# Performance work log

Measured on AMD Instinct MI355X. Metric: run time of the kernel, lower is better.

## Reference

```python
import jax, jax.numpy as jnp
import numpy as np

BN_EPS = 1e-5
DIST_EPS = 1e-8


def setup_inputs() -> dict:
    key = jax.random.key(0)
    ks = jax.random.split(key, 8)
    B, N, S = 8, 8192, 2048
    D_unk, D_kn = 128, 256
    inp = {
        "unknown_xyz": jax.random.uniform(ks[0], (B, N, 3), dtype=jnp.float32),
        "known_xyz": jax.random.uniform(ks[1], (B, S, 3), dtype=jnp.float32),
        "unknown_points": jax.random.normal(ks[2], (B, N, D_unk), dtype=jnp.float32),
        "known_points": jax.random.normal(ks[3], (B, S, D_kn), dtype=jnp.float32),
        "W0": jax.random.normal(ks[4], (256, 384), dtype=jnp.float32) * (1.0 / np.sqrt(384)),
        "b0": jnp.zeros((256,), jnp.float32),
        "g0": jnp.ones((256,), jnp.float32),
        "beta0": jnp.zeros((256,), jnp.float32),
        "W1": jax.random.normal(ks[5], (128, 256), dtype=jnp.float32) * (1.0 / np.sqrt(256)),
        "b1": jnp.zeros((128,), jnp.float32),
        "g1": jnp.ones((128,), jnp.float32),
        "beta1": jnp.zeros((128,), jnp.float32),
    }
    return inp


def _three_nn(unknown_xyz, known_xyz):
    # squared pairwise distances [B, N, S]
    d = jnp.sum((unknown_xyz[:, :, None, :] - known_xyz[:, None, :, :]) ** 2, axis=-1)
    neg_top, idx = jax.lax.top_k(-d, 3)  # 3 smallest distances
    return -neg_top, idx  # dists [B,N,3], idx [B,N,3]


def _conv_bn_relu(x, W, b, g, beta):
    # x: [B, N, Cin]; 1x1 Conv1d == per-point linear
    y = jnp.einsum("bnc,oc->bno", x, W) + b
    mean = jnp.mean(y, axis=(0, 1))
    var = jnp.var(y, axis=(0, 1))  # biased, as BatchNorm training forward
    y = g * (y - mean) * jax.lax.rsqrt(var + BN_EPS) + beta
    return jax.nn.relu(y)


def reference(unknown_xyz, known_xyz, unknown_points, known_points,
              W0, b0, g0, beta0, W1, b1, g1, beta1):
    dists, idx = _three_nn(unknown_xyz, known_xyz)
    dist_recip = 1.0 / (dists + DIST_EPS)
    weight = dist_recip / jnp.sum(dist_recip, axis=2, keepdims=True)  # [B,N,3]
    # gather 3 neighbor features: [B,N,3,D_kn]
    gathered = jax.vmap(lambda f, i: f[i])(known_points, idx)
    interpolated = jnp.sum(weight[..., None] * gathered, axis=2)  # [B,N,D_kn]
    x = jnp.concatenate([unknown_points, interpolated], axis=-1)  # [B,N,384]
    x = _conv_bn_relu(x, W0, b0, g0, beta0)
    x = _conv_bn_relu(x, W1, b1, g1, beta1)
    return x  # [B, N, 128]
```

## Files before the change

kernel.cpp:

```cpp
#include <hip/hip_runtime.h>
#include <hip/hip_bf16.h>


typedef __attribute__((ext_vector_type(8))) short short8;
typedef __attribute__((ext_vector_type(4))) float f32x4;

#define BB 8
#define NN 8192
#define SS 2048
#define M_TOT (BB * NN)
#define N1DIM 256
#define K2DIM 256
#define N2DIM 128
#define BK 64

#define GDIM 5
#define NCELL (GDIM * GDIM * GDIM)
#define SLOTS 32
#define CELLW 0.2f

#define KEY_MASK 0xFFFFF800u
#define IDX_MASK 0x7FFu

__device__ __forceinline__ unsigned short f2bf(float f) {
    unsigned int x = __float_as_uint(f);
    unsigned int r = x + 0x7fffu + ((x >> 16) & 1u);
    return (unsigned short)(r >> 16);
}
__device__ __forceinline__ float bf2f(unsigned short u) {
    return __uint_as_float(((unsigned int)u) << 16);
}
__device__ __forceinline__ unsigned int med3_u32(unsigned int a, unsigned int b,
                                                 unsigned int c) {
    unsigned int r;
    asm("v_med3_u32 %0, %1, %2, %3" : "=v"(r) : "v"(a), "v"(b), "v"(c));
    return r;
}

__device__ __forceinline__ void ins5(unsigned int k[5], unsigned int key) {
    unsigned int n1 = med3_u32(k[0], k[1], key);
    unsigned int n2 = med3_u32(k[1], k[2], key);
    unsigned int n3 = med3_u32(k[2], k[3], key);
    unsigned int n4 = med3_u32(k[3], k[4], key);
    k[0] = min(k[0], key);
    k[1] = n1; k[2] = n2; k[3] = n3; k[4] = n4;
}

__device__ __forceinline__ float rescue_write(
    const unsigned int k[5], float qx, float qy, float qz,
    const float4* __restrict__ kpB, uint4* __restrict__ widx, size_t pt)
{
    unsigned long long e[5];
#pragma unroll
    for (int i = 0; i < 5; ++i) {
        if ((k[i] & KEY_MASK) >= 0x7F800000u) {
            e[i] = 0xFFFFFFFFFFFFFFFFull;
        } else {
            unsigned int idx = k[i] & IDX_MASK;
            float4 c = kpB[idx];
            float dx = c.x - qx, dy = c.y - qy, dz = c.z - qz;
            float d = fmaf(dx, dx, fmaf(dy, dy, dz * dz));
            e[i] = ((unsigned long long)__float_as_uint(d) << 32) | idx;
        }
    }
#pragma unroll
    for (int i = 0; i < 3; ++i)
#pragma unroll
        for (int j = i + 1; j < 5; ++j)
            if (e[j] < e[i]) { unsigned long long t = e[i]; e[i] = e[j]; e[j] = t; }

    float d0 = __uint_as_float((unsigned int)(e[0] >> 32));
    float d1 = __uint_as_float((unsigned int)(e[1] >> 32));
    float d2 = __uint_as_float((unsigned int)(e[2] >> 32));
    float r0 = 1.0f / (d0 + 1e-8f);
    float r1 = 1.0f / (d1 + 1e-8f);
    float r2 = 1.0f / (d2 + 1e-8f);
    float rs = 1.0f / (r0 + r1 + r2);
    unsigned int i0 = (unsigned int)(e[0] & IDX_MASK);
    unsigned int i1 = (unsigned int)(e[1] & IDX_MASK);
    unsigned int i2 = (unsigned int)(e[2] & IDX_MASK);
    widx[pt] = make_uint4(__float_as_uint(r0 * rs), __float_as_uint(r1 * rs),
                          i0 | (i1 << 16), i2);
    return d2;
}

__device__ __forceinline__ void gload_lds16(const void* g, void* lds) {
    __builtin_amdgcn_global_load_lds(
        (const __attribute__((address_space(1))) unsigned int*)g,
        (__attribute__((address_space(3))) unsigned int*)lds, 16, 0, 0);
}

__global__ __launch_bounds__(256) void cvt_w_kernel(
    const float* __restrict__ W0, const float* __restrict__ W1,
    const float* __restrict__ kxyz,
    unsigned short* __restrict__ Wa, unsigned short* __restrict__ Wb,
    unsigned short* __restrict__ Wb1, float4* __restrict__ kpack,
    float4* __restrict__ table, int* __restrict__ cnt,
    int* __restrict__ nfail, float* __restrict__ statsF)
{
    int i = blockIdx.x * 256 + threadIdx.x;
    if (blockIdx.x == 0) {
        for (int j = threadIdx.x; j < 4608; j += 256) statsF[j] = 0.0f;
        if (threadIdx.x == 0) *nfail = 0;
    }
    if (i < BB * NCELL) cnt[i] = 0;
    if (i < BB * NCELL * SLOTS)
        table[i] = make_float4(1e30f, 1e30f, 1e30f, 0.0f);
    if (i < 256 * 384) {
        int o = i / 384, c = i - o * 384;
        unsigned short v = f2bf(W0[i]);
        if (c < 128) Wa[o * 128 + c] = v;
        else         Wb[o * 256 + (c - 128)] = v;
    }
    if (i < N2DIM * K2DIM) Wb1[i] = f2bf(W1[i]);
    if (i < BB * SS) {
        const float* p = kxyz + (size_t)i * 3;
        float px = p[0], py = p[1], pz = p[2];
        kpack[i] = make_float4(px, py, pz, fmaf(px, px, fmaf(py, py, pz * pz)));
    }
}

__global__ __launch_bounds__(256) void bin_scatter_kernel(
    const float* __restrict__ kxyz, float4* __restrict__ table,
    int* __restrict__ cnt)
{
    int i = blockIdx.x * 256 + threadIdx.x;
    if (i >= BB * SS) return;
    int b = i >> 11, s = i & 2047;
    const float* p = kxyz + (size_t)i * 3;
    float x = p[0], y = p[1], z = p[2];
    int cx = min((int)(x * GDIM), GDIM - 1);
    int cy = min((int)(y * GDIM), GDIM - 1);
    int cz = min((int)(z * GDIM), GDIM - 1);
    int cell = (cz * GDIM + cy) * GDIM + cx;
    int slot = atomicAdd(&cnt[b * NCELL + cell], 1);
    if (slot < SLOTS)
        table[((size_t)(b * NCELL + cell)) * SLOTS + slot] =
            make_float4(x, y, z, __int_as_float(s));
}

__global__ __launch_bounds__(256) void nn_grid_kernel(
    const float* __restrict__ uxyz, const float4* __restrict__ table,
    const int* __restrict__ cnt, const float4* __restrict__ kpack,
    uint4* __restrict__ widx, int* __restrict__ fail_list,
    int* __restrict__ nfail)
{
    const int t  = blockIdx.x * 256 + threadIdx.x;
    const int qd = t & 3;
    const size_t pt = (size_t)(t >> 2);
    const int b = (int)(pt >> 13);

    const float* up = uxyz + pt * 3;
    const float qx = up[0], qy = up[1], qz = up[2];

    const int cx = min((int)(qx * GDIM), GDIM - 1);
    const int cy = min((int)(qy * GDIM), GDIM - 1);
    const int cz = min((int)(qz * GDIM), GDIM - 1);
    const float fx = qx * GDIM - cx, fy = qy * GDIM - cy, fz = qz * GDIM - cz;
    int ox = cx - (fx <= 0.5f ? 1 : 0); ox = max(0, min(ox, GDIM - 2));
    int oy = cy - (fy <= 0.5f ? 1 : 0); oy = max(0, min(oy, GDIM - 2));
    int oz = cz - (fz <= 0.5f ? 1 : 0); oz = max(0, min(oz, GDIM - 2));

    const float4* tb = table + (size_t)b * NCELL * SLOTS;
    const int* cb = cnt + b * NCELL;

    unsigned int k[5] = {0xFFFFFFFFu, 0xFFFFFFFFu, 0xFFFFFFFFu,
                         0xFFFFFFFFu, 0xFFFFFFFFu};
    int ovf = 0;
#pragma unroll
    for (int jj = 0; jj < 2; ++jj) {
        const int j = qd * 2 + jj;
        const int dx = j & 1, dy = (j >> 1) & 1, dz = j >> 2;
        const int cell = ((oz + dz) * GDIM + (oy + dy)) * GDIM + (ox + dx);
        ovf |= (cb[cell] > SLOTS) ? 1 : 0;
        const float4* cp = tb + (size_t)cell * SLOTS;
#pragma unroll 8
        for (int s = 0; s < SLOTS; ++s) {
            float4 c = cp[s];
            float ddx = c.x - qx, ddy = c.y - qy, ddz = c.z - qz;
            float d = fmaf(ddx, ddx, fmaf(ddy, ddy, ddz * ddz));
            unsigned int key = (__float_as_uint(d) & KEY_MASK) |
                               (unsigned int)__float_as_int(c.w);
            ins5(k, key);
        }
    }

#pragma unroll
    for (int m = 1; m <= 2; m <<= 1) {
        unsigned int f0 = (unsigned int)__shfl_xor((int)k[0], m);
        unsigned int f1 = (unsigned int)__shfl_xor((int)k[1], m);
        unsigned int f2 = (unsigned int)__shfl_xor((int)k[2], m);
        unsigned int f3 = (unsigned int)__shfl_xor((int)k[3], m);
        unsigned int f4 = (unsigned int)__shfl_xor((int)k[4], m);
        ovf |= __shfl_xor(ovf, m);
        ins5(k, f0); ins5(k, f1); ins5(k, f2); ins5(k, f3); ins5(k, f4);
    }

    if (qd != 0) return;

    float d3 = rescue_write(k, qx, qy, qz, kpack + (size_t)b * SS, widx, pt);

    float lx = ox * CELLW, rx = (ox + 2) * CELLW;
    float ly = oy * CELLW, ry = (oy + 2) * CELLW;
    float lz = oz * CELLW, rz = (oz + 2) * CELLW;
    float covx = fminf(ox == 0 ? 1e30f : qx - lx, ox == GDIM - 2 ? 1e30f : rx - qx);
    float covy = fminf(oy == 0 ? 1e30f : qy - ly, oy == GDIM - 2 ? 1e30f : ry - qy);
    float covz = fminf(oz == 0 ? 1e30f : qz - lz, oz == GDIM - 2 ? 1e30f : rz - qz);
    float g = fminf(covx, fminf(covy, covz));

    if (ovf || !(d3 <= g * g)) {
        int pos = atomicAdd(nfail, 1);
        fail_list[pos] = (int)pt;
    }
}

__global__ __launch_bounds__(256) void nn_brute_kernel(
    const float* __restrict__ uxyz, const float4* __restrict__ kpack,
    const int* __restrict__ fail_list, const int* __restrict__ nfail,
    uint4* __restrict__ widx)
{
    const int l = threadIdx.x & 63;
    const int wv = (blockIdx.x * 256 + threadIdx.x) >> 6;
    const int nw = (gridDim.x * 256) >> 6;
    const int n = *nfail;

    for (int q = wv; q < n; q += nw) {
        const size_t pt = (size_t)fail_list[q];
        const int b = (int)(pt >> 13);
        const float* up = uxyz + pt * 3;
        const float qx = up[0], qy = up[1], qz = up[2];
        const float4* kp = kpack + (size_t)b * SS;

        unsigned int k[5] = {0xFFFFFFFFu, 0xFFFFFFFFu, 0xFFFFFFFFu,
                             0xFFFFFFFFu, 0xFFFFFFFFu};
#pragma unroll 4
        for (int s = l; s < SS; s += 64) {
            float4 c = kp[s];
            float ddx = c.x - qx, ddy = c.y - qy, ddz = c.z - qz;
            float d = fmaf(ddx, ddx, fmaf(ddy, ddy, ddz * ddz));
            unsigned int key = (__float_as_uint(d) & KEY_MASK) | (unsigned int)s;
            ins5(k, key);
        }
#pragma unroll
        for (int m = 1; m <= 32; m <<= 1) {
            unsigned int f0 = (unsigned int)__shfl_xor((int)k[0], m);
            unsigned int f1 = (unsigned int)__shfl_xor((int)k[1], m);
            unsigned int f2 = (unsigned int)__shfl_xor((int)k[2], m);
            unsigned int f3 = (unsigned int)__shfl_xor((int)k[3], m);
            unsigned int f4 = (unsigned int)__shfl_xor((int)k[4], m);
            ins5(k, f0); ins5(k, f1); ins5(k, f2); ins5(k, f3); ins5(k, f4);
        }
        if (l == 0)
            rescue_write(k, qx, qy, qz, kp, widx, pt);
    }
}

__global__ __launch_bounds__(512, 4) void zgemm_kernel(
    const float* __restrict__ kpts,
    const unsigned short* __restrict__ Wb,
    unsigned short* __restrict__ Z)
{
    __shared__ __align__(128) unsigned char smem[2 * 32768];

    const int tid = threadIdx.x;
    const int l = tid & 63, w = tid >> 6;
    const int wm = w >> 2, wn = w & 3;
    const int mt = blockIdx.x >> 1, nh = blockIdx.x & 1;
    const int row0 = mt * 128;
    const int srow = l >> 3, sbo = (l & 7) * 16;
    const int lr = tid >> 2, lcq = tid & 3;

    f32x4 acc[4][2];
#pragma unroll
    for (int m = 0; m < 4; ++m)
#pragma unroll
        for (int n = 0; n < 2; ++n) {
            f32x4 z = {0.f, 0.f, 0.f, 0.f};
            acc[m][n] = z;
        }

    const unsigned char* Bb = (const unsigned char*)Wb + (size_t)nh * 128 * 512;
    float4 af0, af1, af2, af3;

    auto issueA = [&](int t) {
        const float* src = kpts + (size_t)(row0 + lr) * 256 + t * 64 + lcq * 16;
        af0 = ((const float4*)src)[0];
        af1 = ((const float4*)src)[1];
        af2 = ((const float4*)src)[2];
        af3 = ((const float4*)src)[3];
    };
    auto stageB = [&](int buf, int t) {
        unsigned char* Bl = smem + buf * 32768 + 16384;
#pragma unroll
        for (int i = 0; i < 2; ++i) {
            const int r = w * 16 + i * 8 + srow;
            gload_lds16(Bb + (size_t)r * 512 + t * 128 + (sbo ^ ((r & 7) << 4)),
                        Bl + r * 128 + sbo);
        }
    };
    auto xformA = [&](int buf) {
        unsigned char* Al = smem + buf * 32768;
        short8 o0, o1;
        o0[0] = (short)f2bf(af0.x); o0[1] = (short)f2bf(af0.y);
        o0[2] = (short)f2bf(af0.z); o0[3] = (short)f2bf(af0.w);
        o0[4] = (short)f2bf(af1.x); o0[5] = (short)f2bf(af1.y);
        o0[6] = (short)f2bf(af1.z); o0[7] = (short)f2bf(af1.w);
        o1[0] = (short)f2bf(af2.x); o1[1] = (short)f2bf(af2.y);
        o1[2] = (short)f2bf(af2.z); o1[3] = (short)f2bf(af2.w);
        o1[4] = (short)f2bf(af3.x); o1[5] = (short)f2bf(af3.y);
        o1[6] = (short)f2bf(af3.z); o1[7] = (short)f2bf(af3.w);
        const int bo = lcq * 32;
        *(short8*)(Al + lr * 128 + ((bo) ^ ((lr & 7) << 4))) = o0;
        *(short8*)(Al + lr * 128 + ((bo + 16) ^ ((lr & 7) << 4))) = o1;
    };
    auto compute = [&](int buf) {
        const unsigned char* Al = smem + buf * 32768;
        const unsigned char* Bl = Al + 16384;
#pragma unroll
        for (int ks = 0; ks < 2; ++ks) {
            const int bo = ks * 64 + (l >> 4) * 16;
            short8 a[4], bq[2];
#pragma unroll
            for (int m = 0; m < 4; ++m) {
                const int r = wm * 64 + m * 16 + (l & 15);
                a[m] = *(const short8*)(Al + r * 128 + (bo ^ ((r & 7) << 4)));
            }
#pragma unroll
            for (int n = 0; n < 2; ++n) {
                const int r = wn * 32 + n * 16 + (l & 15);
                bq[n] = *(const short8*)(Bl + r * 128 + (bo ^ ((r & 7) << 4)));
            }
#pragma unroll
            for (int m = 0; m < 4; ++m)
#pragma unroll
                for (int n = 0; n < 2; ++n)
                    acc[m][n] = __builtin_amdgcn_mfma_f32_16x16x32_bf16(
                        a[m], bq[n], acc[m][n], 0, 0, 0);
        }
    };

    issueA(0);
    stageB(0, 0);
    xformA(0);
    __syncthreads();
#pragma unroll
    for (int t = 0; t < 4; ++t) {
        const int cur = t & 1;
        if (t + 1 < 4) { issueA(t + 1); stageB(cur ^ 1, t + 1); }
        compute(cur);
        if (t + 1 < 4) xformA(cur ^ 1);
        __syncthreads();
    }

#pragma unroll
    for (int m = 0; m < 4; ++m) {
        const int row = row0 + wm * 64 + m * 16 + (l >> 4) * 4;
#pragma unroll
        for (int n = 0; n < 2; ++n) {
            const int col = nh * 128 + wn * 32 + n * 16 + (l & 15);
            f32x4 v = acc[m][n];
#pragma unroll
            for (int r = 0; r < 4; ++r)
                Z[(size_t)(row + r) * 256 + col] = f2bf(v[r]);
        }
    }
}

__global__ __launch_bounds__(512, 4) void gemm1u_kernel(
    const float* __restrict__ upts,
    const unsigned short* __restrict__ Wa,
    unsigned short* __restrict__ Y0u)
{
    __shared__ __align__(128) unsigned char smem[65536];

    const int tid = threadIdx.x;
    const int l = tid & 63, w = tid >> 6;
    const int wm = w >> 2, wn = w & 3;
    const int mt = blockIdx.x >> 1, nh = blockIdx.x & 1;
    const int row0 = mt * 128;
    const int srow = l >> 3, sbo = (l & 7) * 16;
    const int lr = tid >> 2, lcq = tid & 3;

    {
        const unsigned char* Bb = (const unsigned char*)Wa + (size_t)nh * 128 * 256;
#pragma unroll
        for (int h = 0; h < 2; ++h)
#pragma unroll
            for (int i = 0; i < 2; ++i) {
                const int r = w * 16 + i * 8 + srow;
                gload_lds16(Bb + (size_t)r * 256 + h * 128 + (sbo ^ ((r & 7) << 4)),
                            smem + 32768 + h * 16384 + r * 128 + sbo);
            }
    }
    {
        const float* src = upts + (size_t)(row0 + lr) * 128 + lcq * 32;
        float4 f[8];
#pragma unroll
        for (int q = 0; q < 8; ++q) f[q] = ((const float4*)src)[q];
        unsigned char* Ah = smem + (lcq >> 1) * 16384;
        const int cb = (lcq & 1) * 64;
#pragma unroll
        for (int q = 0; q < 4; ++q) {
            float4 fa = f[q * 2], fb = f[q * 2 + 1];
            short8 o;
            o[0] = (short)f2bf(fa.x); o[1] = (short)f2bf(fa.y);
            o[2] = (short)f2bf(fa.z); o[3] = (short)f2bf(fa.w);
            o[4] = (short)f2bf(fb.x); o[5] = (short)f2bf(fb.y);
            o[6] = (short)f2bf(fb.z); o[7] = (short)f2bf(fb.w);
            *(short8*)(Ah + lr * 128 + ((cb + q * 16) ^ ((lr & 7) << 4))) = o;
        }
    }
    __syncthreads();

    f32x4 acc[4][2];
#pragma unroll
    for (int m = 0; m < 4; ++m)
#pragma unroll
        for (int n = 0; n < 2; ++n) {
            f32x4 z = {0.f, 0.f, 0.f, 0.f};
            acc[m][n] = z;
        }
#pragma unroll
    for (int ks = 0; ks < 4; ++ks) {
        const unsigned char* Al = smem + (ks >> 1) * 16384;
        const unsigned char* Bl = smem + 32768 + (ks >> 1) * 16384;
        const int bo = (ks & 1) * 64 + (l >> 4) * 16;
        short8 a[4], bq[2];
#pragma unroll
        for (int m = 0; m < 4; ++m) {
            const int r = wm * 64 + m * 16 + (l & 15);
            a[m] = *(const short8*)(Al + r * 128 + (bo ^ ((r & 7) << 4)));
        }
#pragma unroll
        for (int n = 0; n < 2; ++n) {
            const int r = wn * 32 + n * 16 + (l & 15);
            bq[n] = *(const short8*)(Bl + r * 128 + (bo ^ ((r & 7) << 4)));
        }
#pragma unroll
        for (int m = 0; m < 4; ++m)
#pragma unroll
            for (int n = 0; n < 2; ++n)
                acc[m][n] = __builtin_amdgcn_mfma_f32_16x16x32_bf16(
                    a[m], bq[n], acc[m][n], 0, 0, 0);
    }

    __syncthreads();
    {
        unsigned short* st = (unsigned short*)smem;
#pragma unroll
        for (int m = 0; m < 4; ++m)
#pragma unroll
            for (int n = 0; n < 2; ++n)
#pragma unroll
                for (int r = 0; r < 4; ++r) {
                    const int row = wm * 64 + m * 16 + (l >> 4) * 4 + r;
                    const int col = wn * 32 + n * 16 + (l & 15);
                    st[row * 136 + col] = f2bf(acc[m][n][r]);
                }
    }
    __syncthreads();
    {
        const int row = tid >> 2, cb = (tid & 3) * 32;
        const unsigned short* st = (const unsigned short*)smem;
        unsigned short* dst = Y0u + (size_t)(row0 + row) * 256 + nh * 128 + cb;
#pragma unroll
        for (int i = 0; i < 4; ++i)
            *(short8*)(dst + i * 8) = *(const short8*)(st + row * 136 + cb + i * 8);
    }
}

__global__ __launch_bounds__(256) void interp_y0_kernel(
    const uint4* __restrict__ widx,
    const unsigned short* __restrict__ Z,
    const unsigned short* __restrict__ Y0u,
    unsigned short* __restrict__ Y0,
    float* __restrict__ statsR)
{
    __shared__ int   sidx[64][3];
    __shared__ float sw[64][3];
    __shared__ float sst[4][512];

    const int tid = threadIdx.x;
    const int bid = blockIdx.x;
    const int b   = bid & 7;
    const int pn  = (bid >> 3) * 64;
    const int wv = tid >> 6, lane = tid & 63;

    if (tid < 64) {
        uint4 wq = widx[(size_t)b * NN + pn + tid];
        float w0 = __uint_as_float(wq.x);
        float w1 = __uint_as_float(wq.y);
        sidx[tid][0] = (int)(wq.z & 0xFFFFu);
        sidx[tid][1] = (int)(wq.z >> 16);
        sidx[tid][2] = (int)wq.w;
        sw[tid][0] = w0; sw[tid][1] = w1; sw[tid][2] = 1.0f - w0 - w1;
    }
    __syncthreads();

    float s1[4] = {0.f, 0.f, 0.f, 0.f}, s2[4] = {0.f, 0.f, 0.f, 0.f};
    const unsigned short* Zb = Z + (size_t)b * SS * 256;
    for (int p = wv; p < 64; p += 4) {
        const int j0 = sidx[p][0], j1 = sidx[p][1], j2 = sidx[p][2];
        const float w0 = sw[p][0], w1 = sw[p][1], w2 = sw[p][2];
        const size_t rb = ((size_t)b * NN + pn + p) * 256 + lane * 4;

        ushort4 z0 = *(const ushort4*)(Zb + (size_t)j0 * 256 + lane * 4);
        ushort4 z1 = *(const ushort4*)(Zb + (size_t)j1 * 256 + lane * 4);
        ushort4 z2 = *(const ushort4*)(Zb + (size_t)j2 * 256 + lane * 4);
        ushort4 u  = *(const ushort4*)(Y0u + rb);

        float f0 = bf2f(u.x) + fmaf(w2, bf2f(z2.x), fmaf(w1, bf2f(z1.x), w0 * bf2f(z0.x)));
        float f1 = bf2f(u.y) + fmaf(w2, bf2f(z2.y), fmaf(w1, bf2f(z1.y), w0 * bf2f(z0.y)));
        float f2v = bf2f(u.z) + fmaf(w2, bf2f(z2.z), fmaf(w1, bf2f(z1.z), w0 * bf2f(z0.z)));
        float f3 = bf2f(u.w) + fmaf(w2, bf2f(z2.w), fmaf(w1, bf2f(z1.w), w0 * bf2f(z0.w)));

        ushort4 o;
        o.x = f2bf(f0); o.y = f2bf(f1); o.z = f2bf(f2v); o.w = f2bf(f3);
        *(ushort4*)(Y0 + rb) = o;

        s1[0] += f0;  s2[0] += f0 * f0;
        s1[1] += f1;  s2[1] += f1 * f1;
        s1[2] += f2v; s2[2] += f2v * f2v;
        s1[3] += f3;  s2[3] += f3 * f3;
    }

#pragma unroll
    for (int j = 0; j < 4; ++j) {
        sst[wv][lane * 4 + j] = s1[j];
        sst[wv][256 + lane * 4 + j] = s2[j];
    }
    __syncthreads();
    {
        float v = sst[0][tid] + sst[1][tid] + sst[2][tid] + sst[3][tid];
        float q = sst[0][256 + tid] + sst[1][256 + tid] +
                  sst[2][256 + tid] + sst[3][256 + tid];
        atomicAdd(&statsR[b * 512 + tid], v);
        atomicAdd(&statsR[b * 512 + 256 + tid], q);
    }
}

#define G2_NT (K2DIM / BK)
__global__ __launch_bounds__(512, 4) void gemm2_kernel(
    const unsigned short* __restrict__ Y0,
    const unsigned short* __restrict__ Wb,
    const float* __restrict__ statsR,
    const float* __restrict__ g0,
    const float* __restrict__ beta0,
    unsigned short* __restrict__ Y1,
    float* __restrict__ stats)
{
    __shared__ __align__(128) unsigned char smem[2 * 32768];
    __shared__ float sgm[K2DIM], sga[K2DIM];

    const int tid = threadIdx.x;
    const int l = tid & 63, w = tid >> 6;
    const int wm = w >> 2, wn = w & 3;
    const int row0 = blockIdx.x * 128;
    const int srow = l >> 3;
    const int sbo  = (l & 7) * 16;
    const int lr  = tid >> 2;
    const int lcq = tid & 3;

    f32x4 acc[4][2];
#pragma unroll
    for (int m = 0; m < 4; ++m)
#pragma unroll
        for (int n = 0; n < 2; ++n) {
            f32x4 z = {0.f, 0.f, 0.f, 0.f};
            acc[m][n] = z;
        }

    const unsigned char* Bb = (const unsigned char*)Wb;
    short8 areg0, areg1;

    auto issueA = [&](int t) {
        const unsigned short* src = Y0 + (size_t)(row0 + lr) * K2DIM + t * BK + lcq * 16;
        areg0 = *(const short8*)src;
        areg1 = *(const short8*)(src + 8);
    };
    auto stageB = [&](int buf, int t) {
        unsigned char* Bl = smem + buf * 32768 + 16384;
        const int k0b = t * (BK * 2);
#pragma unroll
        for (int i = 0; i < 2; ++i) {
            const int r = w * 16 + i * 8 + srow;
            gload_lds16(Bb + (size_t)r * (K2DIM * 2) + k0b + (sbo ^ ((r & 7) << 4)),
                        Bl + r * 128 + sbo);
        }
    };
    auto xformA = [&](int buf, int t) {
        unsigned char* Al = smem + buf * 32768;
        const int kb = t * BK + lcq * 16;
        short8 o0, o1;
#pragma unroll
        for (int j = 0; j < 8; ++j) {
            float f = bf2f((unsigned short)areg0[j]);
            f = fmaxf(fmaf(f, sgm[kb + j], sga[kb + j]), 0.f);
            o0[j] = (short)f2bf(f);
            float g = bf2f((unsigned short)areg1[j]);
            g = fmaxf(fmaf(g, sgm[kb + 8 + j], sga[kb + 8 + j]), 0.f);
            o1[j] = (short)f2bf(g);
        }
        const int bo = lcq * 32;
        *(short8*)(Al + lr * 128 + ((bo) ^ ((lr & 7) << 4))) = o0;
        *(short8*)(Al + lr * 128 + ((bo + 16) ^ ((lr & 7) << 4))) = o1;
    };
    auto compute = [&](int buf) {
        const unsigned char* Al = smem + buf * 32768;
        const unsigned char* Bl = Al + 16384;
#pragma unroll
        for (int ks = 0; ks < 2; ++ks) {
            const int bo = ks * 64 + (l >> 4) * 16;
            short8 a[4], bq[2];
#pragma unroll
            for (int m = 0; m < 4; ++m) {
                const int r = wm * 64 + m * 16 + (l & 15);
                a[m] = *(const short8*)(Al + r * 128 + (bo ^ ((r & 7) << 4)));
            }
#pragma unroll
            for (int n = 0; n < 2; ++n) {
                const int r = wn * 32 + n * 16 + (l & 15);
                bq[n] = *(const short8*)(Bl + r * 128 + (bo ^ ((r & 7) << 4)));
            }
#pragma unroll
            for (int m = 0; m < 4; ++m)
#pragma unroll
                for (int n = 0; n < 2; ++n)
                    acc[m][n] = __builtin_amdgcn_mfma_f32_16x16x32_bf16(
                        a[m], bq[n], acc[m][n], 0, 0, 0);
        }
    };

    if (tid < K2DIM) {
        float s = 0.f, q = 0.f;
#pragma unroll
        for (int r = 0; r < 8; ++r) {
            s += statsR[r * 512 + tid];
            q += statsR[r * 512 + 256 + tid];
        }
        const float inv = 1.0f / (float)M_TOT;
        float mean = s * inv;
        float var  = q * inv - mean * mean;
        float m = g0[tid] * rsqrtf(var + 1e-5f);
        sgm[tid] = m;
        sga[tid] = beta0[tid] - mean * m;
    }
    issueA(0);
    stageB(0, 0);
    __syncthreads();
    xformA(0, 0);
    __syncthreads();

#pragma unroll
    for (int t = 0; t < G2_NT; ++t) {
        const int cur = t & 1;
        if (t + 1 < G2_NT) { issueA(t + 1); stageB(cur ^ 1, t + 1); }
        compute(cur);
        if (t + 1 < G2_NT) xformA(cur ^ 1, t + 1);
        __syncthreads();
    }

    float s1[2] = {0.f, 0.f}, s2[2] = {0.f, 0.f};
#pragma unroll
    for (int m = 0; m < 4; ++m) {
        const int row = row0 + wm * 64 + m * 16 + (l >> 4) * 4;
#pragma unroll
        for (int n = 0; n < 2; ++n) {
            const int col = wn * 32 + n * 16 + (l & 15);
            f32x4 v = acc[m][n];
#pragma unroll
            for (int r = 0; r < 4; ++r) {
                float f = v[r];
                Y1[(size_t)(row + r) * N2DIM + col] = f2bf(f);
                s1[n] += f;
                s2[n] += f * f;
            }
        }
    }
#pragma unroll
    for (int n = 0; n < 2; ++n) {
        s1[n] += __shfl_xor(s1[n], 16, 64);
        s1[n] += __shfl_xor(s1[n], 32, 64);
        s2[n] += __shfl_xor(s2[n], 16, 64);
        s2[n] += __shfl_xor(s2[n], 32, 64);
    }
    if (l < 16) {
#pragma unroll
        for (int n = 0; n < 2; ++n) {
            const int col = wn * 32 + n * 16 + l;
            atomicAdd(&stats[col], s1[n]);
            atomicAdd(&stats[N2DIM + col], s2[n]);
        }
    }
}

__global__ __launch_bounds__(256) void bn_out_kernel(
    const unsigned short* __restrict__ Y1, const float* __restrict__ stats1,
    const float* __restrict__ g1, const float* __restrict__ beta1,
    float* __restrict__ out)
{
    __shared__ float sgm[N2DIM], sga[N2DIM];
    const int tid = threadIdx.x;
    if (tid < N2DIM) {
        const float inv = 1.0f / (float)M_TOT;
        float mean = stats1[tid] * inv;
        float var  = stats1[N2DIM + tid] * inv - mean * mean;
        float m = g1[tid] * rsqrtf(var + 1e-5f);
        sgm[tid] = m;
        sga[tid] = beta1[tid] - mean * m;
    }
    __syncthreads();

    const int total = M_TOT * N2DIM / 8;
    for (int i = blockIdx.x * 256 + tid; i < total; i += gridDim.x * 256) {
        short8 v = ((const short8*)Y1)[i];
        const int cg = (i & 15) * 8;
        float4 o1, o2;
        o1.x = fmaxf(fmaf(bf2f((unsigned short)v[0]), sgm[cg + 0], sga[cg + 0]), 0.f);
        o1.y = fmaxf(fmaf(bf2f((unsigned short)v[1]), sgm[cg + 1], sga[cg + 1]), 0.f);
        o1.z = fmaxf(fmaf(bf2f((unsigned short)v[2]), sgm[cg + 2], sga[cg + 2]), 0.f);
        o1.w = fmaxf(fmaf(bf2f((unsigned short)v[3]), sgm[cg + 3], sga[cg + 3]), 0.f);
        o2.x = fmaxf(fmaf(bf2f((unsigned short)v[4]), sgm[cg + 4], sga[cg + 4]), 0.f);
        o2.y = fmaxf(fmaf(bf2f((unsigned short)v[5]), sgm[cg + 5], sga[cg + 5]), 0.f);
        o2.z = fmaxf(fmaf(bf2f((unsigned short)v[6]), sgm[cg + 6], sga[cg + 6]), 0.f);
        o2.w = fmaxf(fmaf(bf2f((unsigned short)v[7]), sgm[cg + 7], sga[cg + 7]), 0.f);
        ((float4*)out)[i * 2]     = o1;
        ((float4*)out)[i * 2 + 1] = o2;
    }
}

extern "C" void kernel_launch(void* const* d_in, const int* in_sizes, int n_in,
                              void* d_out, int out_size, void* d_ws, size_t ws_size,
                              hipStream_t stream)
{
    const float* uxyz  = (const float*)d_in[0];
    const float* kxyz  = (const float*)d_in[1];
    const float* upts  = (const float*)d_in[2];
    const float* kpts  = (const float*)d_in[3];
    const float* W0    = (const float*)d_in[4];
    const float* g0    = (const float*)d_in[6];
    const float* beta0 = (const float*)d_in[7];
    const float* W1    = (const float*)d_in[8];
    const float* g1    = (const float*)d_in[10];
    const float* beta1 = (const float*)d_in[11];
    float* out = (float*)d_out;

    char* ws = (char*)d_ws;
    const size_t off_xz = 0;
    const size_t off_y0 = 33554432;
    const size_t off_z  = 67108864;
    const size_t off_w  = 75497472;

    unsigned short* Y0u  = (unsigned short*)(ws + off_xz);
    unsigned short* y1   = (unsigned short*)(ws + off_xz);
    unsigned short* y0   = (unsigned short*)(ws + off_y0);
    float4* table    = (float4*)(ws + off_y0);
    int*    cellcnt  = (int*)(ws + off_y0 + 524288);
    int*    nfail    = (int*)(ws + off_y0 + 528384);
    int*    faillist = (int*)(ws + off_y0 + 532480);
    float4* kpack    = (float4*)(ws + off_y0 + 8388608);
    unsigned short* Zb   = (unsigned short*)(ws + off_z);
    unsigned short* wa   = (unsigned short*)(ws + off_w);
    unsigned short* wb   = (unsigned short*)(ws + off_w + 65536);
    unsigned short* wb1  = (unsigned short*)(ws + off_w + 196608);
    float* F = (float*)(ws + off_w + 262144);
    float* statsR = F;
    float* stats1 = F + 4096;
    uint4* widx = (uint4*)(ws + off_w + 262144 + 18432);

    cvt_w_kernel<<<384, 256, 0, stream>>>(W0, W1, kxyz, wa, wb, wb1, kpack,
                                          table, cellcnt, nfail, F);
    bin_scatter_kernel<<<64, 256, 0, stream>>>(kxyz, table, cellcnt);
    nn_grid_kernel<<<1024, 256, 0, stream>>>(uxyz, table, cellcnt, kpack,
                                             widx, faillist, nfail);
    nn_brute_kernel<<<256, 256, 0, stream>>>(uxyz, kpack, faillist, nfail, widx);
    zgemm_kernel<<<256, 512, 0, stream>>>(kpts, wb, Zb);
    gemm1u_kernel<<<1024, 512, 0, stream>>>(upts, wa, Y0u);
    interp_y0_kernel<<<1024, 256, 0, stream>>>(widx, Zb, Y0u, y0, statsR);
    gemm2_kernel<<<512, 512, 0, stream>>>(y0, wb1, statsR, g0, beta0, y1, stats1);
    bn_out_kernel<<<2048, 256, 0, stream>>>(y1, stats1, g1, beta1, out);
}
```

Before: 151.5 us.

## Merge grid NN search and both input GEMMs into one block-dispatched kernel

Three independent stages (grid nearest-neighbour search, known-point Z GEMM, unknown-point GEMM) now run as one launch, with each stage assigned a range of block IDs. The NN search moves from 256-thread blocks to 512-thread blocks. The brute-force fallback runs after the merged kernel and its grid shrinks to 64 blocks. The aim is to cut launch gaps and let the ALU-bound NN work overlap with the MFMA GEMMs. In exchange, the fused kernel carries the launch bounds and 64KB of shared memory for all blocks, which may limit occupancy for the NN blocks.

Result: faster. 145.2 us, median of 3 (-4.1%).

```diff
diff --git a/kernel.cpp b/kernel.cpp
--- a/kernel.cpp
+++ b/kernel.cpp
@@ -139,78 +139,292 @@
             make_float4(x, y, z, __int_as_float(s));
 }
 
-__global__ __launch_bounds__(256) void nn_grid_kernel(
+#define NNB 512
+#define ZB  256
+#define G1B 1024
+__global__ __launch_bounds__(512, 4) void mid_kernel(
     const float* __restrict__ uxyz, const float4* __restrict__ table,
     const int* __restrict__ cnt, const float4* __restrict__ kpack,
     uint4* __restrict__ widx, int* __restrict__ fail_list,
-    int* __restrict__ nfail)
-{
-    const int t  = blockIdx.x * 256 + threadIdx.x;
-    const int qd = t & 3;
-    const size_t pt = (size_t)(t >> 2);
-    const int b = (int)(pt >> 13);
-
-    const float* up = uxyz + pt * 3;
-    const float qx = up[0], qy = up[1], qz = up[2];
-
-    const int cx = min((int)(qx * GDIM), GDIM - 1);
-    const int cy = min((int)(qy * GDIM), GDIM - 1);
-    const int cz = min((int)(qz * GDIM), GDIM - 1);
-    const float fx = qx * GDIM - cx, fy = qy * GDIM - cy, fz = qz * GDIM - cz;
-    int ox = cx - (fx <= 0.5f ? 1 : 0); ox = max(0, min(ox, GDIM - 2));
-    int oy = cy - (fy <= 0.5f ? 1 : 0); oy = max(0, min(oy, GDIM - 2));
-    int oz = cz - (fz <= 0.5f ? 1 : 0); oz = max(0, min(oz, GDIM - 2));
-
-    const float4* tb = table + (size_t)b * NCELL * SLOTS;
-    const int* cb = cnt + b * NCELL;
-
-    unsigned int k[5] = {0xFFFFFFFFu, 0xFFFFFFFFu, 0xFFFFFFFFu,
-                         0xFFFFFFFFu, 0xFFFFFFFFu};
-    int ovf = 0;
-#pragma unroll
-    for (int jj = 0; jj < 2; ++jj) {
-        const int j = qd * 2 + jj;
-        const int dx = j & 1, dy = (j >> 1) & 1, dz = j >> 2;
-        const int cell = ((oz + dz) * GDIM + (oy + dy)) * GDIM + (ox + dx);
-        ovf |= (cb[cell] > SLOTS) ? 1 : 0;
-        const float4* cp = tb + (size_t)cell * SLOTS;
+    int* __restrict__ nfail,
+    const float* __restrict__ kpts, const unsigned short* __restrict__ Wb,
+    unsigned short* __restrict__ Z,
+    const float* __restrict__ upts, const unsigned short* __restrict__ Wa,
+    unsigned short* __restrict__ Y0u)
+{
+    __shared__ __align__(128) unsigned char smem[65536];
+    const int bid = blockIdx.x;
+    const int tid = threadIdx.x;
+
+    if (bid < NNB) {
+        const int t  = bid * 512 + tid;
+        const int qd = t & 3;
+        const size_t pt = (size_t)(t >> 2);
+        const int b = (int)(pt >> 13);
+
+        const float* up = uxyz + pt * 3;
+        const float qx = up[0], qy = up[1], qz = up[2];
+
+        const int cx = min((int)(qx * GDIM), GDIM - 1);
+        const int cy = min((int)(qy * GDIM), GDIM - 1);
+        const int cz = min((int)(qz * GDIM), GDIM - 1);
+        const float fx = qx * GDIM - cx, fy = qy * GDIM - cy, fz = qz * GDIM - cz;
+        int ox = cx - (fx <= 0.5f ? 1 : 0); ox = max(0, min(ox, GDIM - 2));
+        int oy = cy - (fy <= 0.5f ? 1 : 0); oy = max(0, min(oy, GDIM - 2));
+        int oz = cz - (fz <= 0.5f ? 1 : 0); oz = max(0, min(oz, GDIM - 2));
+
+        const float4* tb = table + (size_t)b * NCELL * SLOTS;
+        const int* cb = cnt + b * NCELL;
+
+        unsigned int k[5] = {0xFFFFFFFFu, 0xFFFFFFFFu, 0xFFFFFFFFu,
+                             0xFFFFFFFFu, 0xFFFFFFFFu};
+        int ovf = 0;
+#pragma unroll
+        for (int jj = 0; jj < 2; ++jj) {
+            const int j = qd * 2 + jj;
+            const int dx = j & 1, dy = (j >> 1) & 1, dz = j >> 2;
+            const int cell = ((oz + dz) * GDIM + (oy + dy)) * GDIM + (ox + dx);
+            ovf |= (cb[cell] > SLOTS) ? 1 : 0;
+            const float4* cp = tb + (size_t)cell * SLOTS;
 #pragma unroll 8
-        for (int s = 0; s < SLOTS; ++s) {
-            float4 c = cp[s];
-            float ddx = c.x - qx, ddy = c.y - qy, ddz = c.z - qz;
-            float d = fmaf(ddx, ddx, fmaf(ddy, ddy, ddz * ddz));
-            unsigned int key = (__float_as_uint(d) & KEY_MASK) |
-                               (unsigned int)__float_as_int(c.w);
-            ins5(k, key);
-        }
-    }
-
-#pragma unroll
-    for (int m = 1; m <= 2; m <<= 1) {
-        unsigned int f0 = (unsigned int)__shfl_xor((int)k[0], m);
-        unsigned int f1 = (unsigned int)__shfl_xor((int)k[1], m);
-        unsigned int f2 = (unsigned int)__shfl_xor((int)k[2], m);
-        unsigned int f3 = (unsigned int)__shfl_xor((int)k[3], m);
-        unsigned int f4 = (unsigned int)__shfl_xor((int)k[4], m);
-        ovf |= __shfl_xor(ovf, m);
-        ins5(k, f0); ins5(k, f1); ins5(k, f2); ins5(k, f3); ins5(k, f4);
-    }
-
-    if (qd != 0) return;
-
-    float d3 = rescue_write(k, qx, qy, qz, kpack + (size_t)b * SS, widx, pt);
-
-    float lx = ox * CELLW, rx = (ox + 2) * CELLW;
-    float ly = oy * CELLW, ry = (oy + 2) * CELLW;
-    float lz = oz * CELLW, rz = (oz + 2) * CELLW;
-    float covx = fminf(ox == 0 ? 1e30f : qx - lx, ox == GDIM - 2 ? 1e30f : rx - qx);
-    float covy = fminf(oy == 0 ? 1e30f : qy - ly, oy == GDIM - 2 ? 1e30f : ry - qy);
-    float covz = fminf(oz == 0 ? 1e30f : qz - lz, oz == GDIM - 2 ? 1e30f : rz - qz);
-    float g = fminf(covx, fminf(covy, covz));
-
-    if (ovf || !(d3 <= g * g)) {
-        int pos = atomicAdd(nfail, 1);
-        fail_list[pos] = (int)pt;
+            for (int s = 0; s < SLOTS; ++s) {
+                float4 c = cp[s];
+                float ddx = c.x - qx, ddy = c.y - qy, ddz = c.z - qz;
+                float d = fmaf(ddx, ddx, fmaf(ddy, ddy, ddz * ddz));
+                unsigned int key = (__float_as_uint(d) & KEY_MASK) |
+                                   (unsigned int)__float_as_int(c.w);
+                ins5(k, key);
+            }
+        }
+
+#pragma unroll
+        for (int m = 1; m <= 2; m <<= 1) {
+            unsigned int f0 = (unsigned int)__shfl_xor((int)k[0], m);
+            unsigned int f1 = (unsigned int)__shfl_xor((int)k[1], m);
+            unsigned int f2 = (unsigned int)__shfl_xor((int)k[2], m);
+            unsigned int f3 = (unsigned int)__shfl_xor((int)k[3], m);
+            unsigned int f4 = (unsigned int)__shfl_xor((int)k[4], m);
+            ovf |= __shfl_xor(ovf, m);
+            ins5(k, f0); ins5(k, f1); ins5(k, f2); ins5(k, f3); ins5(k, f4);
+        }
+
+        if (qd != 0) return;
+
+        float d3 = rescue_write(k, qx, qy, qz, kpack + (size_t)b * SS, widx, pt);
+
+        float lx = ox * CELLW, rx = (ox + 2) * CELLW;
+        float ly = oy * CELLW, ry = (oy + 2) * CELLW;
+        float lz = oz * CELLW, rz = (oz + 2) * CELLW;
+        float covx = fminf(ox == 0 ? 1e30f : qx - lx, ox == GDIM - 2 ? 1e30f : rx - qx);
+        float covy = fminf(oy == 0 ? 1e30f : qy - ly, oy == GDIM - 2 ? 1e30f : ry - qy);
+        float covz = fminf(oz == 0 ? 1e30f : qz - lz, oz == GDIM - 2 ? 1e30f : rz - qz);
+        float g = fminf(covx, fminf(covy, covz));
+
+        if (ovf || !(d3 <= g * g)) {
+            int pos = atomicAdd(nfail, 1);
+            fail_list[pos] = (int)pt;
+        }
+        return;
+    }
+
+    const int l = tid & 63, w = tid >> 6;
+    const int wm = w >> 2, wn = w & 3;
+    const int srow = l >> 3, sbo = (l & 7) * 16;
+    const int lr = tid >> 2, lcq = tid & 3;
+
+    if (bid < NNB + ZB) {
+        const int vb = bid - NNB;
+        const int mt = vb >> 1, nh = vb & 1;
+        const int row0 = mt * 128;
+
+        f32x4 acc[4][2];
+#pragma unroll
+        for (int m = 0; m < 4; ++m)
+#pragma unroll
+            for (int n = 0; n < 2; ++n) {
+                f32x4 z = {0.f, 0.f, 0.f, 0.f};
+                acc[m][n] = z;
+            }
+
+        const unsigned char* Bb = (const unsigned char*)Wb + (size_t)nh * 128 * 512;
+        float4 af0, af1, af2, af3;
+
+        auto issueA = [&](int t) {
+            const float* src = kpts + (size_t)(row0 + lr) * 256 + t * 64 + lcq * 16;
+            af0 = ((const float4*)src)[0];
+            af1 = ((const float4*)src)[1];
+            af2 = ((const float4*)src)[2];
+            af3 = ((const float4*)src)[3];
+        };
+        auto stageB = [&](int buf, int t) {
+            unsigned char* Bl = smem + buf * 32768 + 16384;
+#pragma unroll
+            for (int i = 0; i < 2; ++i) {
+                const int r = w * 16 + i * 8 + srow;
+                gload_lds16(Bb + (size_t)r * 512 + t * 128 + (sbo ^ ((r & 7) << 4)),
+                            Bl + r * 128 + sbo);
+            }
+        };
+        auto xformA = [&](int buf) {
+            unsigned char* Al = smem + buf * 32768;
+            short8 o0, o1;
+            o0[0] = (short)f2bf(af0.x); o0[1] = (short)f2bf(af0.y);
+            o0[2] = (short)f2bf(af0.z); o0[3] = (short)f2bf(af0.w);
+            o0[4] = (short)f2bf(af1.x); o0[5] = (short)f2bf(af1.y);
+            o0[6] = (short)f2bf(af1.z); o0[7] = (short)f2bf(af1.w);
+            o1[0] = (short)f2bf(af2.x); o1[1] = (short)f2bf(af2.y);
+            o1[2] = (short)f2bf(af2.z); o1[3] = (short)f2bf(af2.w);
+            o1[4] = (short)f2bf(af3.x); o1[5] = (short)f2bf(af3.y);
+            o1[6] = (short)f2bf(af3.z); o1[7] = (short)f2bf(af3.w);
+            const int bo = lcq * 32;
+            *(short8*)(Al + lr * 128 + ((bo) ^ ((lr & 7) << 4))) = o0;
+            *(short8*)(Al + lr * 128 + ((bo + 16) ^ ((lr & 7) << 4))) = o1;
+        };
+        auto compute = [&](int buf) {
+            const unsigned char* Al = smem + buf * 32768;
+            const unsigned char* Bl = Al + 16384;
+#pragma unroll
+            for (int ks = 0; ks < 2; ++ks) {
+                const int bo = ks * 64 + (l >> 4) * 16;
+                short8 a[4], bq[2];
+#pragma unroll
+                for (int m = 0; m < 4; ++m) {
+                    const int r = wm * 64 + m * 16 + (l & 15);
+                    a[m] = *(const short8*)(Al + r * 128 + (bo ^ ((r & 7) << 4)));
+                }
+#pragma unroll
+                for (int n = 0; n < 2; ++n) {
+                    const int r = wn * 32 + n * 16 + (l & 15);
+                    bq[n] = *(const short8*)(Bl + r * 128 + (bo ^ ((r & 7) << 4)));
+                }
+#pragma unroll
+                for (int m = 0; m < 4; ++m)
+#pragma unroll
+                    for (int n = 0; n < 2; ++n)
+                        acc[m][n] = __builtin_amdgcn_mfma_f32_16x16x32_bf16(
+                            a[m], bq[n], acc[m][n], 0, 0, 0);
+            }
+        };
+
+        issueA(0);
+        stageB(0, 0);
+        xformA(0);
+        __syncthreads();
+#pragma unroll
+        for (int t = 0; t < 4; ++t) {
+            const int cur = t & 1;
+            if (t + 1 < 4) { issueA(t + 1); stageB(cur ^ 1, t + 1); }
+            compute(cur);
+            if (t + 1 < 4) xformA(cur ^ 1);
+            __syncthreads();
+        }
+
+#pragma unroll
+        for (int m = 0; m < 4; ++m) {
+            const int row = row0 + wm * 64 + m * 16 + (l >> 4) * 4;
+#pragma unroll
+            for (int n = 0; n < 2; ++n) {
+                const int col = nh * 128 + wn * 32 + n * 16 + (l & 15);
+                f32x4 v = acc[m][n];
+#pragma unroll
+                for (int r = 0; r < 4; ++r)
+                    Z[(size_t)(row + r) * 256 + col] = f2bf(v[r]);
+            }
+        }
+        return;
+    }
+
+    {
+        const int vb = bid - (NNB + ZB);
+        const int mt = vb >> 1, nh = vb & 1;
+        const int row0 = mt * 128;
+
+        {
+            const unsigned char* Bb = (const unsigned char*)Wa + (size_t)nh * 128 * 256;
+#pragma unroll
+            for (int h = 0; h < 2; ++h)
+#pragma unroll
+                for (int i = 0; i < 2; ++i) {
+                    const int r = w * 16 + i * 8 + srow;
+                    gload_lds16(Bb + (size_t)r * 256 + h * 128 + (sbo ^ ((r & 7) << 4)),
+                                smem + 32768 + h * 16384 + r * 128 + sbo);
+                }
+        }
+        {
+            const float* src = upts + (size_t)(row0 + lr) * 128 + lcq * 32;
+            float4 f[8];
+#pragma unroll
+            for (int q = 0; q < 8; ++q) f[q] = ((const float4*)src)[q];
+            unsigned char* Ah = smem + (lcq >> 1) * 16384;
+            const int cb = (lcq & 1) * 64;
+#pragma unroll
+            for (int q = 0; q < 4; ++q) {
+                float4 fa = f[q * 2], fb = f[q * 2 + 1];
+                short8 o;
+                o[0] = (short)f2bf(fa.x); o[1] = (short)f2bf(fa.y);
+                o[2] = (short)f2bf(fa.z); o[3] = (short)f2bf(fa.w);
+                o[4] = (short)f2bf(fb.x); o[5] = (short)f2bf(fb.y);
+                o[6] = (short)f2bf(fb.z); o[7] = (short)f2bf(fb.w);
+                *(short8*)(Ah + lr * 128 + ((cb + q * 16) ^ ((lr & 7) << 4))) = o;
+            }
+        }
+        __syncthreads();
+
+        f32x4 acc[4][2];
+#pragma unroll
+        for (int m = 0; m < 4; ++m)
+#pragma unroll
+            for (int n = 0; n < 2; ++n) {
+                f32x4 z = {0.f, 0.f, 0.f, 0.f};
+                acc[m][n] = z;
+            }
+#pragma unroll
+        for (int ks = 0; ks < 4; ++ks) {
+            const unsigned char* Al = smem + (ks >> 1) * 16384;
+            const unsigned char* Bl = smem + 32768 + (ks >> 1) * 16384;
+            const int bo = (ks & 1) * 64 + (l >> 4) * 16;
+            short8 a[4], bq[2];
+#pragma unroll
+            for (int m = 0; m < 4; ++m) {
+                const int r = wm * 64 + m * 16 + (l & 15);
+                a[m] = *(const short8*)(Al + r * 128 + (bo ^ ((r & 7) << 4)));
+            }
+#pragma unroll
+            for (int n = 0; n < 2; ++n) {
+                const int r = wn * 32 + n * 16 + (l & 15);
+                bq[n] = *(const short8*)(Bl + r * 128 + (bo ^ ((r & 7) << 4)));
+            }
+#pragma unroll
+            for (int m = 0; m < 4; ++m)
+#pragma unroll
+                for (int n = 0; n < 2; ++n)
+                    acc[m][n] = __builtin_amdgcn_mfma_f32_16x16x32_bf16(
+                        a[m], bq[n], acc[m][n], 0, 0, 0);
+        }
+
+        __syncthreads();
+        {
+            unsigned short* st = (unsigned short*)smem;
+#pragma unroll
+            for (int m = 0; m < 4; ++m)
+#pragma unroll
+                for (int n = 0; n < 2; ++n)
+#pragma unroll
+                    for (int r = 0; r < 4; ++r) {
+                        const int row = wm * 64 + m * 16 + (l >> 4) * 4 + r;
+                        const int col = wn * 32 + n * 16 + (l & 15);
+                        st[row * 136 + col] = f2bf(acc[m][n][r]);
+                    }
+        }
+        __syncthreads();
+        {
+            const int row = tid >> 2, cb = (tid & 3) * 32;
+            const unsigned short* st = (const unsigned short*)smem;
+            unsigned short* dst = Y0u + (size_t)(row0 + row) * 256 + nh * 128 + cb;
+#pragma unroll
+            for (int i = 0; i < 4; ++i)
+                *(short8*)(dst + i * 8) = *(const short8*)(st + row * 136 + cb + i * 8);
+        }
     }
 }
 
@@ -252,220 +466,6 @@
         }
         if (l == 0)
             rescue_write(k, qx, qy, qz, kp, widx, pt);
-    }
-}
-
-__global__ __launch_bounds__(512, 4) void zgemm_kernel(
-    const float* __restrict__ kpts,
-    const unsigned short* __restrict__ Wb,
-    unsigned short* __restrict__ Z)
-{
-    __shared__ __align__(128) unsigned char smem[2 * 32768];
-
-    const int tid = threadIdx.x;
-    const int l = tid & 63, w = tid >> 6;
-    const int wm = w >> 2, wn = w & 3;
-    const int mt = blockIdx.x >> 1, nh = blockIdx.x & 1;
-    const int row0 = mt * 128;
-    const int srow = l >> 3, sbo = (l & 7) * 16;
-    const int lr = tid >> 2, lcq = tid & 3;
-
-    f32x4 acc[4][2];
-#pragma unroll
-    for (int m = 0; m < 4; ++m)
-#pragma unroll
-        for (int n = 0; n < 2; ++n) {
-            f32x4 z = {0.f, 0.f, 0.f, 0.f};
-            acc[m][n] = z;
-        }
-
-    const unsigned char* Bb = (const unsigned char*)Wb + (size_t)nh * 128 * 512;
-    float4 af0, af1, af2, af3;
-
-    auto issueA = [&](int t) {
-        const float* src = kpts + (size_t)(row0 + lr) * 256 + t * 64 + lcq * 16;
-        af0 = ((const float4*)src)[0];
-        af1 = ((const float4*)src)[1];
-        af2 = ((const float4*)src)[2];
-        af3 = ((const float4*)src)[3];
-    };
-    auto stageB = [&](int buf, int t) {
-        unsigned char* Bl = smem + buf * 32768 + 16384;
-#pragma unroll
-        for (int i = 0; i < 2; ++i) {
-            const int r = w * 16 + i * 8 + srow;
-            gload_lds16(Bb + (size_t)r * 512 + t * 128 + (sbo ^ ((r & 7) << 4)),
-                        Bl + r * 128 + sbo);
-        }
-    };
-    auto xformA = [&](int buf) {
-        unsigned char* Al = smem + buf * 32768;
-        short8 o0, o1;
-        o0[0] = (short)f2bf(af0.x); o0[1] = (short)f2bf(af0.y);
-        o0[2] = (short)f2bf(af0.z); o0[3] = (short)f2bf(af0.w);
-        o0[4] = (short)f2bf(af1.x); o0[5] = (short)f2bf(af1.y);
-        o0[6] = (short)f2bf(af1.z); o0[7] = (short)f2bf(af1.w);
-        o1[0] = (short)f2bf(af2.x); o1[1] = (short)f2bf(af2.y);
-        o1[2] = (short)f2bf(af2.z); o1[3] = (short)f2bf(af2.w);
-        o1[4] = (short)f2bf(af3.x); o1[5] = (short)f2bf(af3.y);
-        o1[6] = (short)f2bf(af3.z); o1[7] = (short)f2bf(af3.w);
-        const int bo = lcq * 32;
-        *(short8*)(Al + lr * 128 + ((bo) ^ ((lr & 7) << 4))) = o0;
-        *(short8*)(Al + lr * 128 + ((bo + 16) ^ ((lr & 7) << 4))) = o1;
-    };
-    auto compute = [&](int buf) {
-        const unsigned char* Al = smem + buf * 32768;
-        const unsigned char* Bl = Al + 16384;
-#pragma unroll
-        for (int ks = 0; ks < 2; ++ks) {
-            const int bo = ks * 64 + (l >> 4) * 16;
-            short8 a[4], bq[2];
-#pragma unroll
-            for (int m = 0; m < 4; ++m) {
-                const int r = wm * 64 + m * 16 + (l & 15);
-                a[m] = *(const short8*)(Al + r * 128 + (bo ^ ((r & 7) << 4)));
-            }
-#pragma unroll
-            for (int n = 0; n < 2; ++n) {
-                const int r = wn * 32 + n * 16 + (l & 15);
-                bq[n] = *(const short8*)(Bl + r * 128 + (bo ^ ((r & 7) << 4)));
-            }
-#pragma unroll
-            for (int m = 0; m < 4; ++m)
-#pragma unroll
-                for (int n = 0; n < 2; ++n)
-                    acc[m][n] = __builtin_amdgcn_mfma_f32_16x16x32_bf16(
-                        a[m], bq[n], acc[m][n], 0, 0, 0);
-        }
-    };
-
-    issueA(0);
-    stageB(0, 0);
-    xformA(0);
-    __syncthreads();
-#pragma unroll
-    for (int t = 0; t < 4; ++t) {
-        const int cur = t & 1;
-        if (t + 1 < 4) { issueA(t + 1); stageB(cur ^ 1, t + 1); }
-        compute(cur);
-        if (t + 1 < 4) xformA(cur ^ 1);
-        __syncthreads();
-    }
-
-#pragma unroll
-    for (int m = 0; m < 4; ++m) {
-        const int row = row0 + wm * 64 + m * 16 + (l >> 4) * 4;
-#pragma unroll
-        for (int n = 0; n < 2; ++n) {
-            const int col = nh * 128 + wn * 32 + n * 16 + (l & 15);
-            f32x4 v = acc[m][n];
-#pragma unroll
-            for (int r = 0; r < 4; ++r)
-                Z[(size_t)(row + r) * 256 + col] = f2bf(v[r]);
-        }
-    }
-}
-
-__global__ __launch_bounds__(512, 4) void gemm1u_kernel(
-    const float* __restrict__ upts,
-    const unsigned short* __restrict__ Wa,
-    unsigned short* __restrict__ Y0u)
-{
-    __shared__ __align__(128) unsigned char smem[65536];
-
-    const int tid = threadIdx.x;
-    const int l = tid & 63, w = tid >> 6;
-    const int wm = w >> 2, wn = w & 3;
-    const int mt = blockIdx.x >> 1, nh = blockIdx.x & 1;
-    const int row0 = mt * 128;
-    const int srow = l >> 3, sbo = (l & 7) * 16;
-    const int lr = tid >> 2, lcq = tid & 3;
-
-    {
-        const unsigned char* Bb = (const unsigned char*)Wa + (size_t)nh * 128 * 256;
-#pragma unroll
-        for (int h = 0; h < 2; ++h)
-#pragma unroll
-            for (int i = 0; i < 2; ++i) {
-                const int r = w * 16 + i * 8 + srow;
-                gload_lds16(Bb + (size_t)r * 256 + h * 128 + (sbo ^ ((r & 7) << 4)),
-                            smem + 32768 + h * 16384 + r * 128 + sbo);
-            }
-    }
-    {
-        const float* src = upts + (size_t)(row0 + lr) * 128 + lcq * 32;
-        float4 f[8];
-#pragma unroll
-        for (int q = 0; q < 8; ++q) f[q] = ((const float4*)src)[q];
-        unsigned char* Ah = smem + (lcq >> 1) * 16384;
-        const int cb = (lcq & 1) * 64;
-#pragma unroll
-        for (int q = 0; q < 4; ++q) {
-            float4 fa = f[q * 2], fb = f[q * 2 + 1];
-            short8 o;
-            o[0] = (short)f2bf(fa.x); o[1] = (short)f2bf(fa.y);
-            o[2] = (short)f2bf(fa.z); o[3] = (short)f2bf(fa.w);
-            o[4] = (short)f2bf(fb.x); o[5] = (short)f2bf(fb.y);
-            o[6] = (short)f2bf(fb.z); o[7] = (short)f2bf(fb.w);
-            *(short8*)(Ah + lr * 128 + ((cb + q * 16) ^ ((lr & 7) << 4))) = o;
-        }
-    }
-    __syncthreads();
-
-    f32x4 acc[4][2];
-#pragma unroll
-    for (int m = 0; m < 4; ++m)
-#pragma unroll
-        for (int n = 0; n < 2; ++n) {
-            f32x4 z = {0.f, 0.f, 0.f, 0.f};
-            acc[m][n] = z;
-        }
-#pragma unroll
-    for (int ks = 0; ks < 4; ++ks) {
-        const unsigned char* Al = smem + (ks >> 1) * 16384;
-        const unsigned char* Bl = smem + 32768 + (ks >> 1) * 16384;
-        const int bo = (ks & 1) * 64 + (l >> 4) * 16;
-        short8 a[4], bq[2];
-#pragma unroll
-        for (int m = 0; m < 4; ++m) {
-            const int r = wm * 64 + m * 16 + (l & 15);
-            a[m] = *(const short8*)(Al + r * 128 + (bo ^ ((r & 7) << 4)));
-        }
-#pragma unroll
-        for (int n = 0; n < 2; ++n) {
-            const int r = wn * 32 + n * 16 + (l & 15);
-            bq[n] = *(const short8*)(Bl + r * 128 + (bo ^ ((r & 7) << 4)));
-        }
-#pragma unroll
-        for (int m = 0; m < 4; ++m)
-#pragma unroll
-            for (int n = 0; n < 2; ++n)
-                acc[m][n] = __builtin_amdgcn_mfma_f32_16x16x32_bf16(
-                    a[m], bq[n], acc[m][n], 0, 0, 0);
-    }
-
-    __syncthreads();
-    {
-        unsigned short* st = (unsigned short*)smem;
-#pragma unroll
-        for (int m = 0; m < 4; ++m)
-#pragma unroll
-            for (int n = 0; n < 2; ++n)
-#pragma unroll
-                for (int r = 0; r < 4; ++r) {
-                    const int row = wm * 64 + m * 16 + (l >> 4) * 4 + r;
-                    const int col = wn * 32 + n * 16 + (l & 15);
-                    st[row * 136 + col] = f2bf(acc[m][n][r]);
-                }
-    }
-    __syncthreads();
-    {
-        const int row = tid >> 2, cb = (tid & 3) * 32;
-        const unsigned short* st = (const unsigned short*)smem;
-        unsigned short* dst = Y0u + (size_t)(row0 + row) * 256 + nh * 128 + cb;
-#pragma unroll
-        for (int i = 0; i < 4; ++i)
-            *(short8*)(dst + i * 8) = *(const short8*)(st + row * 136 + cb + i * 8);
     }
 }
 
@@ -771,11 +771,10 @@
     cvt_w_kernel<<<384, 256, 0, stream>>>(W0, W1, kxyz, wa, wb, wb1, kpack,
                                           table, cellcnt, nfail, F);
     bin_scatter_kernel<<<64, 256, 0, stream>>>(kxyz, table, cellcnt);
-    nn_grid_kernel<<<1024, 256, 0, stream>>>(uxyz, table, cellcnt, kpack,
-                                             widx, faillist, nfail);
-    nn_brute_kernel<<<256, 256, 0, stream>>>(uxyz, kpack, faillist, nfail, widx);
-    zgemm_kernel<<<256, 512, 0, stream>>>(kpts, wb, Zb);
-    gemm1u_kernel<<<1024, 512, 0, stream>>>(upts, wa, Y0u);
+    mid_kernel<<<NNB + ZB + G1B, 512, 0, stream>>>(
+        uxyz, table, cellcnt, kpack, widx, faillist, nfail,
+        kpts, wb, Zb, upts, wa, Y0u);
+    nn_brute_kernel<<<64, 256, 0, stream>>>(uxyz, kpack, faillist, nfail, widx);
     interp_y0_kernel<<<1024, 256, 0, stream>>>(widx, Zb, Y0u, y0, statsR);
     gemm2_kernel<<<512, 512, 0, stream>>>(y0, wb1, statsR, g0, beta0, y1, stats1);
     bn_out_kernel<<<2048, 256, 0, stream>>>(y1, stats1, g1, beta1, out);
```
